# Optimization experiments

Measured on AMD Instinct MI355X. Metric: run time of the kernel, lower is better.

## Reference

```python
import jax, jax.numpy as jnp
import numpy as np

B, H, S, D = 4, 16, 2048, 64


def setup_inputs() -> dict:
    key = jax.random.key(0)
    kq, kk, kv = jax.random.split(key, 3)
    Q = jax.random.normal(kq, (B, H, S, D), dtype=jnp.float32)
    K = jax.random.normal(kk, (B, H, S, D), dtype=jnp.float32)
    V = jax.random.normal(kv, (B, H, S, D), dtype=jnp.float32)
    # causal mask, True = position is masked (torch.masked_fill semantics)
    mask = jnp.triu(jnp.ones((S, S), dtype=bool), k=1)[None, None, :, :]
    return {"Q": Q, "K": K, "V": V, "mask": mask}


def _custom_softmax(x):
    # Faithful to the source: subtract the GLOBAL max of the tensor,
    # then normalize by the row-sum of exps along the last dim.
    x = x - jnp.max(x)
    e = jnp.exp(x)
    return e / jnp.sum(e, axis=-1, keepdims=True)


def reference(Q, K, V, mask):
    head_dim = jnp.asarray(K.shape[-1], dtype=Q.dtype)
    # scores: [B, H, S_q, S_k]
    scores = jnp.einsum("bhqd,bhkd->bhqk", Q, K) / jnp.sqrt(head_dim)
    scores = jnp.where(mask, -jnp.inf, scores)
    attn = _custom_softmax(scores)
    # p_drop = 0.0 -> dropout branch skipped in original
    out = jnp.einsum("bhqk,bhkd->bhqd", attn, V)
    return out
```

## Files before the change

kernel.cpp:

```cpp
#include <hip/hip_runtime.h>

typedef float    f32x4 __attribute__((ext_vector_type(4)));
typedef _Float16 f16x8 __attribute__((ext_vector_type(8)));

constexpr int S_LEN = 2048;
constexpr int DIM   = 64;
constexpr int QBLK  = 128;
constexpr int KBLK  = 64;

#define QSCALE 0.1803368801111f
#define THR    11.5f

__global__ __launch_bounds__(256, 3)
void fattn(const float* __restrict__ Q, const float* __restrict__ K,
           const float* __restrict__ V, float* __restrict__ Out)
{
    __shared__ _Float16 Ks[2][KBLK * DIM];
    __shared__ _Float16 Vt[2][DIM * KBLK];

    const int tid  = threadIdx.x;
    const int lane = tid & 63;
    const int wv   = tid >> 6;
    const int g    = lane >> 4;
    const int c    = lane & 15;

    const int id    = blockIdx.x;
    const int local = id >> 3;
    const int bh    = (id & 7) * 8 + (local & 7);
    const int qt    = 15 - (local >> 3);
    const int qbase = qt * QBLK;
    const int qw    = qbase + wv * 32;
    const int nkt   = 2 * qt + 2;
    const size_t base = (size_t)bh * (S_LEN * DIM);

    f16x8 qf[2][2];
    #pragma unroll
    for (int qh = 0; qh < 2; ++qh) {
        const float* qp = Q + base + (size_t)(qw + qh * 16 + c) * DIM + g * 8;
        #pragma unroll
        for (int dc = 0; dc < 2; ++dc) {
            const f32x4 f0 = *(const f32x4*)(qp + dc * 32);
            const f32x4 f1 = *(const f32x4*)(qp + dc * 32 + 4);
            f16x8 q;
            #pragma unroll
            for (int i = 0; i < 4; ++i) {
                q[i]     = (_Float16)(f0[i] * QSCALE);
                q[i + 4] = (_Float16)(f1[i] * QSCALE);
            }
            qf[dc][qh] = q;
        }
    }

    const int krow = tid >> 3;
    const int kd0  = (tid & 7) * 8;
    const float* Kb = K + base;
    const float* Vb = V + base;

    f32x4 kreg[2][2];
    float vreg[2][8];

#define LOAD_KV(KT)                                                            \
    {                                                                          \
        const int ktb_ = (KT) * KBLK;                                          \
        _Pragma("unroll")                                                      \
        for (int sl = 0; sl < 2; ++sl) {                                       \
            const float* kp = Kb + (size_t)(ktb_ + krow + sl * 32) * DIM + kd0;\
            kreg[sl][0] = *(const f32x4*)kp;                                   \
            kreg[sl][1] = *(const f32x4*)(kp + 4);                             \
            const float* vp = Vb + (size_t)(ktb_ + sl * 32 + wv * 4) * DIM + lane; \
            _Pragma("unroll")                                                  \
            for (int mi = 0; mi < 8; ++mi)                                     \
                vreg[sl][mi] = vp[(size_t)((mi >> 2) * 16 + (mi & 3)) * DIM];  \
        }                                                                      \
    }

#define WRITE_KV(B)                                                            \
    {                                                                          \
        _Pragma("unroll")                                                      \
        for (int sl = 0; sl < 2; ++sl) {                                       \
            const int row = krow + sl * 32;                                    \
            f16x8 kb;                                                          \
            _Pragma("unroll")                                                  \
            for (int i = 0; i < 4; ++i) {                                      \
                kb[i]     = (_Float16)kreg[sl][0][i];                          \
                kb[i + 4] = (_Float16)kreg[sl][1][i];                          \
            }                                                                  \
            *(f16x8*)((char*)Ks[B] + row * 128 + ((kd0 * 2) ^ ((row & 7) << 4))) = kb; \
            f16x8 vb;                                                          \
            _Pragma("unroll")                                                  \
            for (int mi = 0; mi < 8; ++mi) vb[mi] = (_Float16)vreg[sl][mi];    \
            const int oct = wv + sl * 4;                                       \
            *(f16x8*)((char*)Vt[B] + lane * 128 + ((oct * 16) ^ ((lane & 7) << 4))) = vb; \
        }                                                                      \
    }

    f32x4 o[4][2];
    #pragma unroll
    for (int dt = 0; dt < 4; ++dt)
        #pragma unroll
        for (int qh = 0; qh < 2; ++qh) o[dt][qh] = (f32x4){0.f, 0.f, 0.f, 0.f};
    float m[2] = {-INFINITY, -INFINITY};
    float l[2] = {0.f, 0.f};

    LOAD_KV(0)
    WRITE_KV(0)
    LOAD_KV(1)
    __syncthreads();

    for (int kt = 0; kt < nkt; ++kt) {
        const int cur = kt & 1;
        const int ktb = kt * KBLK;
        if (kt + 1 < nkt) WRITE_KV(cur ^ 1)
        if (kt + 2 < nkt) LOAD_KV(kt + 2)

        if (ktb <= qw + 31) {
            f32x4 s[4][2];
            __builtin_amdgcn_s_setprio(1);
            #pragma unroll
            for (int ct = 0; ct < 4; ++ct) {
                const int r = ct * 16 + c;
                const char* kp = (const char*)Ks[cur] + r * 128;
                const f16x8 kf0 = *(const f16x8*)(kp + ((g * 16)      ^ ((r & 7) << 4)));
                const f16x8 kf1 = *(const f16x8*)(kp + ((64 + g * 16) ^ ((r & 7) << 4)));
                #pragma unroll
                for (int qh = 0; qh < 2; ++qh) {
                    f32x4 acc = (f32x4){0.f, 0.f, 0.f, 0.f};
                    acc = __builtin_amdgcn_mfma_f32_16x16x32_f16(kf0, qf[0][qh], acc, 0, 0, 0);
                    acc = __builtin_amdgcn_mfma_f32_16x16x32_f16(kf1, qf[1][qh], acc, 0, 0, 0);
                    s[ct][qh] = acc;
                }
            }
            __builtin_amdgcn_s_setprio(0);

            if (ktb + KBLK - 1 > qw) {
                #pragma unroll
                for (int ct = 0; ct < 4; ++ct)
                    #pragma unroll
                    for (int qh = 0; qh < 2; ++qh)
                        #pragma unroll
                        for (int r = 0; r < 4; ++r)
                            if (ktb + ct * 16 + g * 4 + r > qw + qh * 16 + c)
                                s[ct][qh][r] = -INFINITY;
            }

            float rm[2];
            #pragma unroll
            for (int qh = 0; qh < 2; ++qh) {
                float v = s[0][qh][0];
                #pragma unroll
                for (int ct = 0; ct < 4; ++ct)
                    #pragma unroll
                    for (int r = 0; r < 4; ++r) v = fmaxf(v, s[ct][qh][r]);
                v = fmaxf(v, __shfl_xor(v, 16));
                v = fmaxf(v, __shfl_xor(v, 32));
                rm[qh] = v;
            }
            const float need = fmaxf(rm[0] - m[0], rm[1] - m[1]);
            if (!__all(need <= THR)) {
                #pragma unroll
                for (int qh = 0; qh < 2; ++qh) {
                    const float mn = fmaxf(m[qh], rm[qh]);
                    const float sc = __builtin_amdgcn_exp2f(m[qh] - mn);
                    m[qh] = mn;
                    l[qh] *= sc;
                    #pragma unroll
                    for (int dt = 0; dt < 4; ++dt)
                        #pragma unroll
                        for (int r = 0; r < 4; ++r) o[dt][qh][r] *= sc;
                }
            }
            float rs[2] = {0.f, 0.f};
            #pragma unroll
            for (int ct = 0; ct < 4; ++ct)
                #pragma unroll
                for (int qh = 0; qh < 2; ++qh)
                    #pragma unroll
                    for (int r = 0; r < 4; ++r) {
                        const float pv = __builtin_amdgcn_exp2f(s[ct][qh][r] - m[qh]);
                        s[ct][qh][r] = pv;
                        rs[qh] += pv;
                    }
            #pragma unroll
            for (int qh = 0; qh < 2; ++qh) {
                float v = rs[qh];
                v += __shfl_xor(v, 16);
                v += __shfl_xor(v, 32);
                l[qh] += v;
            }

            f16x8 pa[2][2];
            #pragma unroll
            for (int qh = 0; qh < 2; ++qh)
                #pragma unroll
                for (int kc = 0; kc < 2; ++kc) {
                    f16x8 pk;
                    #pragma unroll
                    for (int r = 0; r < 4; ++r) {
                        pk[r]     = (_Float16)s[2 * kc][qh][r];
                        pk[r + 4] = (_Float16)s[2 * kc + 1][qh][r];
                    }
                    pa[qh][kc] = pk;
                }

            __builtin_amdgcn_s_setprio(1);
            #pragma unroll
            for (int dt = 0; dt < 4; ++dt) {
                const int dd = dt * 16 + c;
                const char* vp = (const char*)Vt[cur] + dd * 128;
                #pragma unroll
                for (int kc = 0; kc < 2; ++kc) {
                    const f16x8 vf = *(const f16x8*)(vp +
                        ((kc * 64 + g * 16) ^ ((dd & 7) << 4)));
                    #pragma unroll
                    for (int qh = 0; qh < 2; ++qh)
                        o[dt][qh] = __builtin_amdgcn_mfma_f32_16x16x32_f16(
                            vf, pa[qh][kc], o[dt][qh], 0, 0, 0);
                }
            }
            __builtin_amdgcn_s_setprio(0);
        }
        __syncthreads();
    }

    #pragma unroll
    for (int qh = 0; qh < 2; ++qh) {
        const float invl = 1.f / l[qh];
        const size_t qoff = base + (size_t)(qw + qh * 16 + c) * DIM;
        #pragma unroll
        for (int dt = 0; dt < 4; ++dt) {
            f32x4 ov;
            #pragma unroll
            for (int r = 0; r < 4; ++r) ov[r] = o[dt][qh][r] * invl;
            *(f32x4*)(Out + qoff + dt * 16 + g * 4) = ov;
        }
    }
#undef LOAD_KV
#undef WRITE_KV
}

extern "C" void kernel_launch(void* const* d_in, const int* in_sizes, int n_in,
                              void* d_out, int out_size, void* d_ws, size_t ws_size,
                              hipStream_t stream)
{
    const float* Q = (const float*)d_in[0];
    const float* K = (const float*)d_in[1];
    const float* V = (const float*)d_in[2];
    float* Out = (float*)d_out;
    fattn<<<dim3(1024), 256, 0, stream>>>(Q, K, V, Out);
}
```

Before: 67.06 us.

## Overlap KV tile staging with QK MFMAs and use packed fp16 conversions

```diff
diff --git a/kernel.cpp b/kernel.cpp
--- a/kernel.cpp
+++ b/kernel.cpp
@@ -2,6 +2,7 @@
 
 typedef float    f32x4 __attribute__((ext_vector_type(4)));
 typedef _Float16 f16x8 __attribute__((ext_vector_type(8)));
+typedef __fp16   h16x2 __attribute__((ext_vector_type(2)));
 
 constexpr int S_LEN = 2048;
 constexpr int DIM   = 64;
@@ -11,18 +12,39 @@
 #define QSCALE 0.1803368801111f
 #define THR    11.5f
 
-__global__ __launch_bounds__(256, 3)
+static __device__ __forceinline__ f16x8 pack8(f32x4 a, f32x4 b) {
+    union { h16x2 h[4]; f16x8 v; } u;
+    u.h[0] = __builtin_amdgcn_cvt_pkrtz(a[0], a[1]);
+    u.h[1] = __builtin_amdgcn_cvt_pkrtz(a[2], a[3]);
+    u.h[2] = __builtin_amdgcn_cvt_pkrtz(b[0], b[1]);
+    u.h[3] = __builtin_amdgcn_cvt_pkrtz(b[2], b[3]);
+    return u.v;
+}
+static __device__ __forceinline__ f16x8 pack8f(const float* v) {
+    union { h16x2 h[4]; f16x8 v8; } u;
+    u.h[0] = __builtin_amdgcn_cvt_pkrtz(v[0], v[1]);
+    u.h[1] = __builtin_amdgcn_cvt_pkrtz(v[2], v[3]);
+    u.h[2] = __builtin_amdgcn_cvt_pkrtz(v[4], v[5]);
+    u.h[3] = __builtin_amdgcn_cvt_pkrtz(v[6], v[7]);
+    return u.v8;
+}
+
+__global__ __launch_bounds__(256, 1)
 void fattn(const float* __restrict__ Q, const float* __restrict__ K,
            const float* __restrict__ V, float* __restrict__ Out)
 {
     __shared__ _Float16 Ks[2][KBLK * DIM];
     __shared__ _Float16 Vt[2][DIM * KBLK];
+    __shared__ unsigned ldspad[5120];
 
     const int tid  = threadIdx.x;
     const int lane = tid & 63;
     const int wv   = tid >> 6;
     const int g    = lane >> 4;
     const int c    = lane & 15;
+
+    unsigned pd = ((volatile unsigned*)ldspad)[0];
+    asm volatile("" :: "v"(pd));
 
     const int id    = blockIdx.x;
     const int local = id >> 3;
@@ -41,13 +63,7 @@
         for (int dc = 0; dc < 2; ++dc) {
             const f32x4 f0 = *(const f32x4*)(qp + dc * 32);
             const f32x4 f1 = *(const f32x4*)(qp + dc * 32 + 4);
-            f16x8 q;
-            #pragma unroll
-            for (int i = 0; i < 4; ++i) {
-                q[i]     = (_Float16)(f0[i] * QSCALE);
-                q[i + 4] = (_Float16)(f1[i] * QSCALE);
-            }
-            qf[dc][qh] = q;
+            qf[dc][qh] = pack8(f0 * QSCALE, f1 * QSCALE);
         }
     }
 
@@ -79,16 +95,9 @@
         _Pragma("unroll")                                                      \
         for (int sl = 0; sl < 2; ++sl) {                                       \
             const int row = krow + sl * 32;                                    \
-            f16x8 kb;                                                          \
-            _Pragma("unroll")                                                  \
-            for (int i = 0; i < 4; ++i) {                                      \
-                kb[i]     = (_Float16)kreg[sl][0][i];                          \
-                kb[i + 4] = (_Float16)kreg[sl][1][i];                          \
-            }                                                                  \
+            const f16x8 kb = pack8(kreg[sl][0], kreg[sl][1]);                  \
             *(f16x8*)((char*)Ks[B] + row * 128 + ((kd0 * 2) ^ ((row & 7) << 4))) = kb; \
-            f16x8 vb;                                                          \
-            _Pragma("unroll")                                                  \
-            for (int mi = 0; mi < 8; ++mi) vb[mi] = (_Float16)vreg[sl][mi];    \
+            const f16x8 vb = pack8f(vreg[sl]);                                 \
             const int oct = wv + sl * 4;                                       \
             *(f16x8*)((char*)Vt[B] + lane * 128 + ((oct * 16) ^ ((lane & 7) << 4))) = vb; \
         }                                                                      \
@@ -110,11 +119,10 @@
     for (int kt = 0; kt < nkt; ++kt) {
         const int cur = kt & 1;
         const int ktb = kt * KBLK;
-        if (kt + 1 < nkt) WRITE_KV(cur ^ 1)
-        if (kt + 2 < nkt) LOAD_KV(kt + 2)
-
-        if (ktb <= qw + 31) {
-            f32x4 s[4][2];
+        const bool active = (ktb <= qw + 31);
+
+        f32x4 s[4][2];
+        if (active) {
             __builtin_amdgcn_s_setprio(1);
             #pragma unroll
             for (int ct = 0; ct < 4; ++ct) {
@@ -142,7 +150,12 @@
                             if (ktb + ct * 16 + g * 4 + r > qw + qh * 16 + c)
                                 s[ct][qh][r] = -INFINITY;
             }
-
+        }
+
+        if (kt + 1 < nkt) WRITE_KV(cur ^ 1)
+        if (kt + 2 < nkt) LOAD_KV(kt + 2)
+
+        if (active) {
             float rm[2];
             #pragma unroll
             for (int qh = 0; qh < 2; ++qh) {
@@ -192,15 +205,8 @@
             #pragma unroll
             for (int qh = 0; qh < 2; ++qh)
                 #pragma unroll
-                for (int kc = 0; kc < 2; ++kc) {
-                    f16x8 pk;
-                    #pragma unroll
-                    for (int r = 0; r < 4; ++r) {
-                        pk[r]     = (_Float16)s[2 * kc][qh][r];
-                        pk[r + 4] = (_Float16)s[2 * kc + 1][qh][r];
-                    }
-                    pa[qh][kc] = pk;
-                }
+                for (int kc = 0; kc < 2; ++kc)
+                    pa[qh][kc] = pack8(s[2 * kc][qh], s[2 * kc + 1][qh]);
 
             __builtin_amdgcn_s_setprio(1);
             #pragma unroll
```

Measured after the change: 77.56 us. +15.7%, slower.
